# Optimization experiments

Hardware: AMD Instinct MI355X
Metric: run time of the kernel (lower is better)

The kernel has to match this reference:

```python
import jax, jax.numpy as jnp
import numpy as np

N, E, G, D = 100000, 1600000, 1000, 32
EPS = 1e-5


def setup_inputs() -> dict:
    key = jax.random.key(0)
    ks = jax.random.split(key, 24)
    inp = {
        'h': jax.random.normal(ks[0], (N, D), dtype=jnp.float32),
        'src': jax.random.randint(ks[1], (E,), 0, N, dtype=jnp.int32),
        'dst': jax.random.randint(ks[2], (E,), 0, N, dtype=jnp.int32),
        'graph_id': jnp.sort(jax.random.randint(ks[3], (N,), 0, G, dtype=jnp.int32)),
    }
    dims = [D, 32, 32, 32, 1]
    ki = 4
    for i in range(4):
        inp[f'conv_w{i}'] = jax.random.normal(ks[ki], (dims[i], dims[i + 1]), dtype=jnp.float32) * 0.1; ki += 1
        inp[f'conv_b{i}'] = jax.random.normal(ks[ki], (dims[i + 1],), dtype=jnp.float32) * 0.1; ki += 1
        inp[f'bn_g{i}'] = jnp.ones((dims[i + 1],), dtype=jnp.float32)
        inp[f'bn_b{i}'] = jnp.zeros((dims[i + 1],), dtype=jnp.float32)
    mlp_dims = [D + 32 + 32 + 32 + 1, 128, 64, 1]  # 129 -> 128 -> 64 -> 1
    for i in range(3):
        inp[f'mlp_w{i}'] = jax.random.normal(ks[ki], (mlp_dims[i], mlp_dims[i + 1]), dtype=jnp.float32) * 0.1; ki += 1
        inp[f'mlp_b{i}'] = jax.random.normal(ks[ki], (mlp_dims[i + 1],), dtype=jnp.float32) * 0.1; ki += 1
    return inp


def _mean_agg(x, src, dst):
    # DGL update_all(copy_u, mean): h'_v = mean of h_u over in-neighbors u of v
    deg = jax.ops.segment_sum(jnp.ones((src.shape[0],), x.dtype), dst, num_segments=N)
    agg = jax.ops.segment_sum(x[src], dst, num_segments=N)
    return agg / jnp.maximum(deg, 1.0)[:, None]


def _bn(x, g, b):
    # BatchNorm1d in training mode: batch statistics over node dim
    m = x.mean(axis=0)
    v = x.var(axis=0)
    return g * (x - m) * jax.lax.rsqrt(v + EPS) + b


def reference(h, src, dst, graph_id,
              conv_w0, conv_b0, conv_w1, conv_b1, conv_w2, conv_b2, conv_w3, conv_b3,
              bn_g0, bn_b0, bn_g1, bn_b1, bn_g2, bn_b2, bn_g3, bn_b3,
              mlp_w0, mlp_b0, mlp_w1, mlp_b1, mlp_w2, mlp_b2):
    conv = [(conv_w0, conv_b0), (conv_w1, conv_b1), (conv_w2, conv_b2), (conv_w3, conv_b3)]
    bn = [(bn_g0, bn_b0), (bn_g1, bn_b1), (bn_g2, bn_b2), (bn_g3, bn_b3)]
    h_list = [h]
    x = h
    for (w, b), (g, bb) in zip(conv, bn):
        x = _mean_agg(x, src, dst) @ w + b      # GCNConv
        x = jax.nn.relu(_bn(x, g, bb))           # BN + ReLU
        h_list.append(x)
    h_final = jnp.concatenate(h_list, axis=1)    # [N, 129]
    # dgl.mean_nodes: per-graph mean pool
    cnt = jax.ops.segment_sum(jnp.ones((N,), h_final.dtype), graph_id, num_segments=G)
    hg = jax.ops.segment_sum(h_final, graph_id, num_segments=G) / jnp.maximum(cnt, 1.0)[:, None]
    hg = jax.nn.relu(hg @ mlp_w0 + mlp_b0)
    hg = jax.nn.relu(hg @ mlp_w1 + mlp_b1)
    hg = hg @ mlp_w2 + mlp_b2
    return hg.reshape(-1)                         # [G]
```

## Files before the change

kernel.cpp:

```cpp
#include <hip/hip_runtime.h>

#define NSLOT 32
#define BN_EPS 1e-5f
#define NSB 256
#define BKBITS 8
#define BKN 256
#define MAXBUCK 512

static inline int cdiv_h(int a, int b) { return (a + b - 1) / b; }

__device__ __forceinline__ float4 f4add(float4 a, float4 b) {
    return make_float4(a.x + b.x, a.y + b.y, a.z + b.z, a.w + b.w);
}

__device__ __forceinline__ unsigned bf16rtn(float x) {
    unsigned u = __float_as_uint(x);
    return (u + 0x7FFFu + ((u >> 16) & 1u)) >> 16;
}
__device__ __forceinline__ unsigned bf16pack2(float lo, float hi) {
    return bf16rtn(lo) | (bf16rtn(hi) << 16);
}
__device__ __forceinline__ float bfLO(unsigned u) { return __uint_as_float(u << 16); }
__device__ __forceinline__ float bfHI(unsigned u) { return __uint_as_float(u & 0xFFFF0000u); }

__device__ __forceinline__ int blk_excl_scan256(int v, int t) {
    __shared__ int wsum[4];
    int l = t & 63, w = t >> 6;
    int incl = v;
#pragma unroll
    for (int off = 1; off < 64; off <<= 1) {
        int o = __shfl_up(incl, off, 64);
        if (l >= off) incl += o;
    }
    if (l == 63) wsum[w] = incl;
    __syncthreads();
    int wofs = 0;
#pragma unroll
    for (int i = 0; i < 4; i++) wofs += (i < w) ? wsum[i] : 0;
    __syncthreads();
    return wofs + incl - v;
}

__device__ __forceinline__ void bn_coef(const float* __restrict__ sSum, const float* __restrict__ sSq,
                                        const float* __restrict__ bg, const float* __restrict__ bb,
                                        float invN, int ch, float* aOut, float* cOut) {
    float S = 0.f, Q = 0.f;
#pragma unroll
    for (int s = 0; s < NSLOT; s++) { S += sSum[s * 32 + ch]; Q += sSq[s * 32 + ch]; }
    float m = S * invN;
    float var = Q * invN - m * m;
    if (var < 0.f) var = 0.f;
    float iv = rsqrtf(var + BN_EPS);
    float a = bg[ch] * iv;
    *aOut = a;
    *cOut = bb[ch] - m * a;
}

__device__ __forceinline__ void inline_scan512(const int* __restrict__ tot, int* __restrict__ sOut,
                                               int* __restrict__ sTot, int nbuck, int t) {
    int v0 = (t < nbuck) ? tot[t] : 0;
    int v1 = (256 + t < nbuck) ? tot[256 + t] : 0;
    int e0 = blk_excl_scan256(v0, t);
    if (t == 255) *sTot = e0 + v0;
    __syncthreads();
    int e1 = blk_excl_scan256(v1, t) + *sTot;
    sOut[t] = e0;
    sOut[256 + t] = e1;
    __syncthreads();
}

__device__ __forceinline__ void accPlain(float* dst, uint4 v) {
    dst[0] += bfLO(v.x); dst[1] += bfHI(v.x);
    dst[2] += bfLO(v.y); dst[3] += bfHI(v.y);
    dst[4] += bfLO(v.z); dst[5] += bfHI(v.z);
    dst[6] += bfLO(v.w); dst[7] += bfHI(v.w);
}
__device__ __forceinline__ void accAff(float* dst, uint4 v, const float* a8, const float* c8) {
    float x[8] = { bfLO(v.x), bfHI(v.x), bfLO(v.y), bfHI(v.y),
                   bfLO(v.z), bfHI(v.z), bfLO(v.w), bfHI(v.w) };
#pragma unroll
    for (int q = 0; q < 8; q++) { float r = fmaf(a8[q], x[q], c8[q]); dst[q] += r > 0.f ? r : 0.f; }
}

struct KArgs {
    const float* h; const int* src; const int* dst; const int* gid;
    const float* W0; const float* b0c; const float* W1; const float* b1c;
    const float* W2; const float* b2c; const float* w3; const float* b3c;
    const float* bg0; const float* bb0; const float* bg1; const float* bb1;
    const float* bg2; const float* bb2; const float* bg3; const float* bb3;
    const float* mw0; const float* mb0; const float* mw1; const float* mb1;
    const float* mw2; const float* mb2;
    int* histT; int* prefixB; int* totalP; int* totalU;
    unsigned* ebuf; uint4* hb; int* col; int* rs; int* re; int* gstart;
    uint4* y0b; uint4* y1b; uint4* y2b; float* y3;
    float* sSum; float* sSq; float* out;
    int N, E, G, nbuck, chunk, NT64, NT256;
    float invN;
};


__global__ __launch_bounds__(256) void k_p1(KArgs a) {
    __shared__ int bins[MAXBUCK];
    int t = threadIdx.x, bid = blockIdx.x;
    if (bid < NSB) {
        if (bid == 0) {
            for (int i = t; i < 4 * NSLOT * 32; i += 256) { a.sSum[i] = 0.f; a.sSq[i] = 0.f; }
        }
        for (int b = t; b < a.nbuck; b += 256) bins[b] = 0;
        __syncthreads();
        int lo = bid * a.chunk, hi = lo + a.chunk; if (hi > a.E) hi = a.E;
        for (int i = lo + t; i < hi; i += 256) atomicAdd(&bins[a.dst[i] >> BKBITS], 1);
        __syncthreads();
        for (int b = t; b < a.nbuck; b += 256) a.histT[bid * a.nbuck + b] = bins[b];
    } else {
        int node = (bid - NSB) * 256 + t;
        if (node < a.N) {
            const float4* s4 = (const float4*)a.h + (size_t)node * 8;
            float x[32];
#pragma unroll
            for (int q = 0; q < 8; q++) {
                float4 v = s4[q];
                x[4*q] = v.x; x[4*q+1] = v.y; x[4*q+2] = v.z; x[4*q+3] = v.w;
            }
            uint4* d4 = a.hb + (size_t)node * 4;
#pragma unroll
            for (int q = 0; q < 4; q++) {
                uint4 o;
                o.x = bf16pack2(x[8*q+0], x[8*q+1]);
                o.y = bf16pack2(x[8*q+2], x[8*q+3]);
                o.z = bf16pack2(x[8*q+4], x[8*q+5]);
                o.w = bf16pack2(x[8*q+6], x[8*q+7]);
                d4[q] = o;
            }
        }
    }
}


__global__ __launch_bounds__(256) void k_p2(KArgs a) {
    int b = blockIdx.x, t = threadIdx.x;
    int i = b * 256 + t;
    if (i < a.N) {
        int g = a.gid[i];
        int gp = (i == 0) ? -1 : a.gid[i - 1];
        for (int x = gp + 1; x <= g; ++x) a.gstart[x] = i;
        if (i == a.N - 1) { for (int x = g + 1; x <= a.G; ++x) a.gstart[x] = a.N; }
    }
    int c = a.histT[t * a.nbuck + b];
    int pad = (c + 15) & ~15;
    int ep = blk_excl_scan256(pad, t);
    a.prefixB[b * NSB + t] = ep;
    int ec = blk_excl_scan256(c, t);
    if (t == NSB - 1) { a.totalP[b] = ep + pad; a.totalU[b] = ec + c; }
}


__global__ __launch_bounds__(256) void k_p3(KArgs a) {
    __shared__ int sBP[512];
    __shared__ int sTot;
    __shared__ int cur[MAXBUCK];
    int bid = blockIdx.x, t = threadIdx.x;
    inline_scan512(a.totalP, sBP, &sTot, a.nbuck, t);
    for (int b = t; b < a.nbuck; b += 256) cur[b] = sBP[b] + a.prefixB[b * NSB + bid];
    __syncthreads();
    int lo = bid * a.chunk, hi = lo + a.chunk; if (hi > a.E) hi = a.E;
    for (int i = lo + t; i < hi; i += 256) {
        int d = a.dst[i], s = a.src[i];
        int b = d >> BKBITS;
        int pos = atomicAdd(&cur[b], 1);
        a.ebuf[pos] = ((unsigned)(d & (BKN - 1)) << 24) | (unsigned)s;
    }
}


__global__ __launch_bounds__(256) void k_p4(KArgs a) {
    __shared__ int sBP[512];
    __shared__ int sTot;
    __shared__ int binCnt[BKN], binStart[BKN], cursor[BKN];
    __shared__ int cellBase[NSB], cellCnt[NSB];
    int b = blockIdx.x, t = threadIdx.x;
    inline_scan512(a.totalP, sBP, &sTot, a.nbuck, t);
    int basePb = sBP[b];
    __syncthreads();
    inline_scan512(a.totalU, sBP, &sTot, a.nbuck, t);
    int baseUb = sBP[b];
    cellBase[t] = basePb + a.prefixB[b * NSB + t];
    cellCnt[t]  = a.histT[t * a.nbuck + b];
    binCnt[t] = 0; cursor[t] = 0;
    __syncthreads();
    {
        int cb = cellBase[t], cc = cellCnt[t];
        for (int j = 0; j < cc; j++) atomicAdd(&binCnt[a.ebuf[cb + j] >> 24], 1);
    }
    __syncthreads();
    int bs = blk_excl_scan256(binCnt[t], t);
    binStart[t] = bs;
    __syncthreads();
    {
        int cb = cellBase[t], cc = cellCnt[t];
        for (int j = 0; j < cc; j++) {
            unsigned e = a.ebuf[cb + j];
            int l = e >> 24;
            int pos = binStart[l] + atomicAdd(&cursor[l], 1);
            a.col[baseUb + pos] = (int)(e & 0xFFFFFFu);
        }
    }
    int node = b * BKN + t;
    if (node < a.N) {
        a.rs[node] = baseUb + binStart[t];
        a.re[node] = baseUb + binStart[t] + binCnt[t];
    }
}


template <bool AFF>
__device__ __forceinline__ void agg_tile(const KArgs& a, int* scol, float (*sW)[32],
                                         float (*sWS)[32], float (*sWQ)[32], int tile, int t,
                                         const uint4* __restrict__ yin, uint4* __restrict__ yout,
                                         const float* __restrict__ bias, const float* a8, const float* c8,
                                         float* __restrict__ oSum, float* __restrict__ oSq) {
    int lane = t & 3, grp = t >> 2;
    int node0 = tile * 64, node = node0 + grp;
    int base0 = 0, len = 0;
    if (node0 < a.N) {
        int last = node0 + 63; if (last > a.N - 1) last = a.N - 1;
        base0 = a.rs[node0];
        len = a.re[last] - base0;
    }
    bool lds = (len > 0 && len <= 2048);
    if (lds) { for (int i = t; i < len; i += 256) scol[i] = a.col[base0 + i]; }
    __syncthreads();

    float accA[8], accB[8];
#pragma unroll
    for (int q = 0; q < 8; q++) { accA[q] = 0.f; accB[q] = 0.f; }
    float vout[8];
#pragma unroll
    for (int q = 0; q < 8; q++) vout[q] = 0.f;
    int s0 = 0, s1 = 0;
    if (node < a.N) {
        s0 = a.rs[node]; s1 = a.re[node];
#define GATH2(vv, c) vv = yin[(size_t)(c) * 4 + lane]
#define DOACC(d, g) do { if (AFF) accAff(d, g, a8, c8); else accPlain(d, g); } while (0)
        const int* idx = lds ? scol : a.col;
        int j = lds ? s0 - base0 : s0;
        int j1 = lds ? s1 - base0 : s1;
        if (j + 4 <= j1) {
            uint4 g0, g1, g2, g3;
            GATH2(g0, idx[j]); GATH2(g1, idx[j + 1]); GATH2(g2, idx[j + 2]); GATH2(g3, idx[j + 3]);
            j += 4;
            for (; j + 4 <= j1; j += 4) {
                uint4 h0, h1, h2, h3;
                GATH2(h0, idx[j]); GATH2(h1, idx[j + 1]); GATH2(h2, idx[j + 2]); GATH2(h3, idx[j + 3]);
                DOACC(accA, g0); DOACC(accB, g1); DOACC(accA, g2); DOACC(accB, g3);
                g0 = h0; g1 = h1; g2 = h2; g3 = h3;
            }
            DOACC(accA, g0); DOACC(accB, g1); DOACC(accA, g2); DOACC(accB, g3);
        }
        for (; j < j1; ++j) { uint4 g; GATH2(g, idx[j]); DOACC(accA, g); }
#undef GATH2
#undef DOACC
    }
    float* sM = (float*)scol;
    __syncthreads();
    if (node < a.N) {
        int deg = s1 - s0;
        float inv = (deg > 0) ? 1.f / (float)deg : 1.f;
#pragma unroll
        for (int q = 0; q < 8; q++) sM[grp * 33 + lane * 8 + q] = (accA[q] + accB[q]) * inv;
    }
    __syncthreads();
    if (node < a.N) {
        const float4* b4 = (const float4*)bias;
        float4 b0 = b4[lane * 2], b1 = b4[lane * 2 + 1];
        float outv[8] = { b0.x, b0.y, b0.z, b0.w, b1.x, b1.y, b1.z, b1.w };
#pragma unroll
        for (int k = 0; k < 32; k++) {
            float mk = sM[grp * 33 + k];
#pragma unroll
            for (int q = 0; q < 8; q++) outv[q] += mk * sW[k][lane * 8 + q];
        }
#pragma unroll
        for (int q = 0; q < 8; q++) vout[q] = outv[q];
        uint4 o;
        o.x = bf16pack2(vout[0], vout[1]);
        o.y = bf16pack2(vout[2], vout[3]);
        o.z = bf16pack2(vout[4], vout[5]);
        o.w = bf16pack2(vout[6], vout[7]);
        yout[(size_t)node * 4 + lane] = o;
    }
    float sqv[8];
#pragma unroll
    for (int q = 0; q < 8; q++) sqv[q] = vout[q] * vout[q];
#pragma unroll
    for (int off = 4; off < 64; off <<= 1) {
#pragma unroll
        for (int q = 0; q < 8; q++) {
            vout[q] += __shfl_xor(vout[q], off, 64);
            sqv[q]  += __shfl_xor(sqv[q],  off, 64);
        }
    }
    int w = t >> 6, l = t & 63;
    if (l < 4) {
#pragma unroll
        for (int q = 0; q < 8; q++) { sWS[w][l * 8 + q] = vout[q]; sWQ[w][l * 8 + q] = sqv[q]; }
    }
    __syncthreads();
    if (t < 32) {
        float S = sWS[0][t] + sWS[1][t] + sWS[2][t] + sWS[3][t];
        float Q = sWQ[0][t] + sWQ[1][t] + sWQ[2][t] + sWQ[3][t];
        int slot = tile & (NSLOT - 1);
        atomicAdd(&oSum[slot * 32 + t], S);
        atomicAdd(&oSq[slot * 32 + t], Q);
    }
}


__global__ __launch_bounds__(256, 4) void k_p5(KArgs a) {
    __shared__ int scol[2112];
    __shared__ float sW[32][32];
    __shared__ float sWS[4][32];
    __shared__ float sWQ[4][32];
    int t = threadIdx.x;
    for (int i = t; i < 1024; i += 256) sW[i >> 5][i & 31] = a.W0[i];
    __syncthreads();
    agg_tile<false>(a, scol, sW, sWS, sWQ, blockIdx.x, t, a.hb, a.y0b, a.b0c, nullptr, nullptr,
                    a.sSum + 0 * NSLOT * 32, a.sSq + 0 * NSLOT * 32);
}


__device__ __forceinline__ void aggF_kernel(const KArgs& a, const uint4* yin, uint4* yout,
                                            const float* W, const float* bias,
                                            const float* pSum, const float* pSq,
                                            const float* bg, const float* bb,
                                            float* oSum, float* oSq) {
    __shared__ int scol[2112];
    __shared__ float sW[32][32];
    __shared__ float sA[32], sC[32];
    __shared__ float sWS[4][32];
    __shared__ float sWQ[4][32];
    int t = threadIdx.x;
    for (int i = t; i < 1024; i += 256) sW[i >> 5][i & 31] = W[i];
    if (t < 32) bn_coef(pSum, pSq, bg, bb, a.invN, t, &sA[t], &sC[t]);
    __syncthreads();
    float a8[8], c8[8];
    int lane = t & 3;
#pragma unroll
    for (int q = 0; q < 8; q++) { a8[q] = sA[lane * 8 + q]; c8[q] = sC[lane * 8 + q]; }
    agg_tile<true>(a, scol, sW, sWS, sWQ, blockIdx.x, t, yin, yout, bias, a8, c8, oSum, oSq);
}

__global__ __launch_bounds__(256, 4) void k_p6(KArgs a) {
    aggF_kernel(a, a.y0b, a.y1b, a.W1, a.b1c,
                a.sSum + 0 * NSLOT * 32, a.sSq + 0 * NSLOT * 32, a.bg0, a.bb0,
                a.sSum + 1 * NSLOT * 32, a.sSq + 1 * NSLOT * 32);
}
__global__ __launch_bounds__(256, 4) void k_p7(KArgs a) {
    aggF_kernel(a, a.y1b, a.y2b, a.W2, a.b2c,
                a.sSum + 1 * NSLOT * 32, a.sSq + 1 * NSLOT * 32, a.bg1, a.bb1,
                a.sSum + 2 * NSLOT * 32, a.sSq + 2 * NSLOT * 32);
}


__global__ __launch_bounds__(256) void k_p8(KArgs a) {
    __shared__ float sw[32], sA[32], sC[32];
    int t = threadIdx.x;
    float* q = (float*)a.hb;
    if (t < 32) {
        sw[t] = a.w3[t];
        bn_coef(a.sSum + 2 * NSLOT * 32, a.sSq + 2 * NSLOT * 32, a.bg2, a.bb2,
                a.invN, t, &sA[t], &sC[t]);
    }
    __syncthreads();
    int i = blockIdx.x * 256 + t;
    if (i < a.N) {
        const uint4* x4 = a.y2b + (size_t)i * 4;
        float acc = 0.f;
#pragma unroll
        for (int qq = 0; qq < 4; qq++) {
            uint4 u = x4[qq];
            float vv[8] = { bfLO(u.x), bfHI(u.x), bfLO(u.y), bfHI(u.y),
                            bfLO(u.z), bfHI(u.z), bfLO(u.w), bfHI(u.w) };
#pragma unroll
            for (int r = 0; r < 8; r++) {
                int k = qq * 8 + r;
                float xv = sA[k] * vv[r] + sC[k];
                xv = xv > 0.f ? xv : 0.f;
                acc += xv * sw[k];
            }
        }
        q[i] = acc;
    }
}


__global__ __launch_bounds__(256) void k_p9(KArgs a) {
    __shared__ float sWS3[4], sWQ3[4];
    const float* q = (const float*)a.hb;
    int t = threadIdx.x;
    int i = blockIdx.x * 256 + t;
    float lsum = 0.f, lsq = 0.f;
    if (i < a.N) {
        int s0 = a.rs[i], s1 = a.re[i];
        float a0 = 0.f, a1 = 0.f, a2 = 0.f, a3 = 0.f;
        int j = s0;
        if (j + 4 <= s1) {
            float g0 = q[a.col[j]], g1 = q[a.col[j+1]], g2 = q[a.col[j+2]], g3 = q[a.col[j+3]];
            j += 4;
            for (; j + 4 <= s1; j += 4) {
                float h0 = q[a.col[j]], h1 = q[a.col[j+1]], h2 = q[a.col[j+2]], h3 = q[a.col[j+3]];
                a0 += g0; a1 += g1; a2 += g2; a3 += g3;
                g0 = h0; g1 = h1; g2 = h2; g3 = h3;
            }
            a0 += g0; a1 += g1; a2 += g2; a3 += g3;
        }
        for (; j < s1; ++j) a0 += q[a.col[j]];
        float acc = (a0 + a1) + (a2 + a3);
        float inv = (s1 > s0) ? 1.f / (float)(s1 - s0) : 1.f;
        float v = acc * inv + a.b3c[0];
        a.y3[i] = v; lsum = v; lsq = v * v;
    }
#pragma unroll
    for (int off = 1; off < 64; off <<= 1) {
        lsum += __shfl_xor(lsum, off, 64);
        lsq  += __shfl_xor(lsq,  off, 64);
    }
    if ((t & 63) == 0) { sWS3[t >> 6] = lsum; sWQ3[t >> 6] = lsq; }
    __syncthreads();
    if (t == 0) {
        float S = sWS3[0] + sWS3[1] + sWS3[2] + sWS3[3];
        float Q = sWQ3[0] + sWQ3[1] + sWQ3[2] + sWQ3[3];
        int slot = blockIdx.x & (NSLOT - 1);
        atomicAdd(&a.sSum[3 * NSLOT * 32 + slot * 32], S);
        atomicAdd(&a.sSq[3 * NSLOT * 32 + slot * 32], Q);
    }
}


__global__ __launch_bounds__(256) void k_p10(KArgs a) {
    __shared__ float pcA[128], pcC[128];
    __shared__ float sP[8][128];
    __shared__ float sY[4];
    __shared__ float hg[129];
    __shared__ float hid1[128];
    __shared__ float hid2[64];
    int g = blockIdx.x;
    int t = threadIdx.x;
    if (t < 97) {
        int layer = (t == 96) ? 3 : (t >> 5);
        int ch = t & 31;
        const float* bg = (layer == 0) ? a.bg0 : (layer == 1) ? a.bg1 : (layer == 2) ? a.bg2 : a.bg3;
        const float* bb = (layer == 0) ? a.bb0 : (layer == 1) ? a.bb1 : (layer == 2) ? a.bb2 : a.bb3;
        bn_coef(a.sSum + layer * NSLOT * 32, a.sSq + layer * NSLOT * 32, bg, bb, a.invN, ch,
                &pcA[t], &pcC[t]);
    }
    __syncthreads();
    int s0 = a.gstart[g], s1 = a.gstart[g + 1];
    int lane = t & 31, slot = t >> 5;
    int arr = lane >> 3, sub = lane & 7;
    const unsigned* yb = (arr == 1) ? (const unsigned*)a.y0b
                       : (arr == 2) ? (const unsigned*)a.y1b : (const unsigned*)a.y2b;
    float4 a4 = make_float4(1.f, 1.f, 1.f, 1.f);
    float4 c4 = make_float4(0.f, 0.f, 0.f, 0.f);
    bool aff = (arr > 0);
    if (aff) {
        a4 = ((const float4*)pcA)[(arr - 1) * 8 + sub];
        c4 = ((const float4*)pcC)[(arr - 1) * 8 + sub];
    }
    float4 acc = make_float4(0.f, 0.f, 0.f, 0.f);
    for (int n = s0 + slot; n < s1; n += 8) {
        float4 v;
        if (arr == 0) {
            v = ((const float4*)a.h)[(size_t)n * 8 + sub];
        } else {
            uint2 u = ((const uint2*)yb)[(size_t)n * 8 + sub];
            v = make_float4(bfLO(u.x), bfHI(u.x), bfLO(u.y), bfHI(u.y));
        }
        if (aff) {
            float vx = fmaf(a4.x, v.x, c4.x); vx = vx > 0.f ? vx : 0.f;
            float vy = fmaf(a4.y, v.y, c4.y); vy = vy > 0.f ? vy : 0.f;
            float vz = fmaf(a4.z, v.z, c4.z); vz = vz > 0.f ? vz : 0.f;
            float vw = fmaf(a4.w, v.w, c4.w); vw = vw > 0.f ? vw : 0.f;
            v = make_float4(vx, vy, vz, vw);
        }
        acc = f4add(acc, v);
    }
    float ys = 0.f;
    {
        float aY = pcA[96], cY = pcC[96];
        for (int n = s0 + t; n < s1; n += 256) {
            float v = fmaf(aY, a.y3[n], cY);
            ys += v > 0.f ? v : 0.f;
        }
    }
#pragma unroll
    for (int off = 1; off < 64; off <<= 1) ys += __shfl_xor(ys, off, 64);
    if ((t & 63) == 0) sY[t >> 6] = ys;
    ((float4*)&sP[slot][lane * 4])[0] = acc;
    __syncthreads();
    float inv = (s1 > s0) ? 1.f / (float)(s1 - s0) : 1.f;
    if (t < 128) {
        float S = 0.f;
#pragma unroll
        for (int s = 0; s < 8; s++) S += sP[s][t];
        hg[t] = S * inv;
    } else if (t == 128) {
        float S = sY[0] + sY[1] + sY[2] + sY[3];
        hg[128] = S * inv;
    }
    __syncthreads();
    if (t < 128) {
        float v = a.mb0[t];
        for (int i = 0; i < 129; i++) v += hg[i] * a.mw0[i * 128 + t];
        hid1[t] = v > 0.f ? v : 0.f;
    }
    __syncthreads();
    if (t < 64) {
        float v = a.mb1[t];
        for (int i = 0; i < 128; i++) v += hid1[i] * a.mw1[i * 64 + t];
        hid2[t] = v > 0.f ? v : 0.f;
    }
    __syncthreads();
    if (t < 64) {
        float v = hid2[t] * a.mw2[t];
        for (int off = 32; off > 0; off >>= 1) v += __shfl_down(v, off, 64);
        if (t == 0) a.out[g] = v + a.mb2[0];
    }
}


extern "C" void kernel_launch(void* const* d_in, const int* in_sizes, int n_in,
                              void* d_out, int out_size, void* d_ws, size_t ws_size,
                              hipStream_t stream) {
    KArgs ka;
    ka.h   = (const float*)d_in[0];
    ka.src = (const int*)d_in[1];
    ka.dst = (const int*)d_in[2];
    ka.gid = (const int*)d_in[3];
    const float* convw[4], *convb[4], *bng[4], *bnb[4];
    for (int i = 0; i < 4; i++) {
        convw[i] = (const float*)d_in[4 + 4 * i];
        convb[i] = (const float*)d_in[5 + 4 * i];
        bng[i]   = (const float*)d_in[6 + 4 * i];
        bnb[i]   = (const float*)d_in[7 + 4 * i];
    }
    ka.W0 = convw[0]; ka.b0c = convb[0]; ka.W1 = convw[1]; ka.b1c = convb[1];
    ka.W2 = convw[2]; ka.b2c = convb[2]; ka.w3 = convw[3]; ka.b3c = convb[3];
    ka.bg0 = bng[0]; ka.bb0 = bnb[0]; ka.bg1 = bng[1]; ka.bb1 = bnb[1];
    ka.bg2 = bng[2]; ka.bb2 = bnb[2]; ka.bg3 = bng[3]; ka.bb3 = bnb[3];
    ka.mw0 = (const float*)d_in[20]; ka.mb0 = (const float*)d_in[21];
    ka.mw1 = (const float*)d_in[22]; ka.mb1 = (const float*)d_in[23];
    ka.mw2 = (const float*)d_in[24]; ka.mb2 = (const float*)d_in[25];

    const int N = in_sizes[0] / 32;
    const int E = in_sizes[1];
    const int G = out_size;
    const int nbuck = cdiv_h(N, BKN);
    const int chunk = cdiv_h(E, NSB);

    char* ws = (char*)d_ws;
    size_t off = 0;
    auto alloc = [&](size_t bytes) -> void* {
        void* p = ws + off;
        off += (bytes + 511) & ~(size_t)511;
        return p;
    };
    ka.histT   = (int*)alloc((size_t)NSB * nbuck * 4);
    ka.prefixB = (int*)alloc((size_t)nbuck * NSB * 4);
    ka.totalP  = (int*)alloc((size_t)nbuck * 4);
    ka.totalU  = (int*)alloc((size_t)nbuck * 4);
    size_t ebufE = (size_t)E + (size_t)16 * NSB * nbuck;
    ka.ebuf = (unsigned*)alloc(ebufE * 4);
    ka.hb   = (uint4*)alloc((size_t)N * 64);
    ka.col  = (int*)alloc((size_t)E * 4);
    ka.rs   = (int*)alloc((size_t)N * 4);
    ka.re   = (int*)alloc((size_t)N * 4);
    ka.gstart = (int*)alloc((size_t)(G + 1) * 4);
    ka.y0b  = (uint4*)alloc((size_t)N * 64);
    ka.y1b  = (uint4*)alloc((size_t)N * 64);
    ka.y2b  = (uint4*)alloc((size_t)N * 64);
    ka.y3   = (float*)alloc((size_t)N * 4);
    ka.sSum = (float*)alloc((size_t)4 * NSLOT * 32 * 4);
    ka.sSq  = (float*)alloc((size_t)4 * NSLOT * 32 * 4);
    ka.out  = (float*)d_out;
    (void)ws_size; (void)n_in;

    ka.N = N; ka.E = E; ka.G = G; ka.nbuck = nbuck; ka.chunk = chunk;
    ka.NT64 = cdiv_h(N, 64); ka.NT256 = cdiv_h(N, 256);
    ka.invN = 1.f / (float)N;

    k_p1<<<NSB + ka.NT256, 256, 0, stream>>>(ka);
    k_p2<<<nbuck, 256, 0, stream>>>(ka);
    k_p3<<<NSB, 256, 0, stream>>>(ka);
    k_p4<<<nbuck, 256, 0, stream>>>(ka);
    k_p5<<<ka.NT64, 256, 0, stream>>>(ka);
    k_p6<<<ka.NT64, 256, 0, stream>>>(ka);
    k_p7<<<ka.NT64, 256, 0, stream>>>(ka);
    k_p8<<<ka.NT256, 256, 0, stream>>>(ka);
    k_p9<<<ka.NT256, 256, 0, stream>>>(ka);
    k_p10<<<G, 256, 0, stream>>>(ka);
}
```

Baseline: 294.6 us.

## Apply first-layer weight before aggregation and specialize layer-0 kernel

Uses linearity of mean aggregation to compute h@W0 per node in the bf16 conversion pass, so the first aggregation kernel only gathers pre-projected features, adds bias and skips its shared-memory matmul. The agg_tile template is inlined into separate kernels, and occupancy hints are raised (layer 0 to 6 blocks, layers 1-2 to 5). This removes a 32x32 matmul and two barriers from the gather-bound layer-0 kernel, at the cost of a per-node matmul in the prep kernel and bf16 rounding applied after the projection instead of before.

```diff
diff --git a/kernel.cpp b/kernel.cpp
--- a/kernel.cpp
+++ b/kernel.cpp
@@ -91,7 +91,7 @@
     const float* mw0; const float* mb0; const float* mw1; const float* mb1;
     const float* mw2; const float* mb2;
     int* histT; int* prefixB; int* totalP; int* totalU;
-    unsigned* ebuf; uint4* hb; int* col; int* rs; int* re; int* gstart;
+    unsigned* ebuf; uint4* pb; int* col; int* rs; int* re; int* gstart;
     uint4* y0b; uint4* y1b; uint4* y2b; float* y3;
     float* sSum; float* sSq; float* out;
     int N, E, G, nbuck, chunk, NT64, NT256;
@@ -101,6 +101,7 @@
 
 __global__ __launch_bounds__(256) void k_p1(KArgs a) {
     __shared__ int bins[MAXBUCK];
+    __shared__ float sW[32][32];
     int t = threadIdx.x, bid = blockIdx.x;
     if (bid < NSB) {
         if (bid == 0) {
@@ -113,25 +114,35 @@
         __syncthreads();
         for (int b = t; b < a.nbuck; b += 256) a.histT[bid * a.nbuck + b] = bins[b];
     } else {
+        for (int i = t; i < 1024; i += 256) sW[i >> 5][i & 31] = a.W0[i];
+        __syncthreads();
         int node = (bid - NSB) * 256 + t;
-        if (node < a.N) {
-            const float4* s4 = (const float4*)a.h + (size_t)node * 8;
-            float x[32];
-#pragma unroll
-            for (int q = 0; q < 8; q++) {
-                float4 v = s4[q];
-                x[4*q] = v.x; x[4*q+1] = v.y; x[4*q+2] = v.z; x[4*q+3] = v.w;
-            }
-            uint4* d4 = a.hb + (size_t)node * 4;
-#pragma unroll
-            for (int q = 0; q < 4; q++) {
-                uint4 o;
-                o.x = bf16pack2(x[8*q+0], x[8*q+1]);
-                o.y = bf16pack2(x[8*q+2], x[8*q+3]);
-                o.z = bf16pack2(x[8*q+4], x[8*q+5]);
-                o.w = bf16pack2(x[8*q+6], x[8*q+7]);
-                d4[q] = o;
-            }
+        if (node >= a.N) return;
+        float x[32];
+        const float4* s4 = (const float4*)a.h + (size_t)node * 8;
+#pragma unroll
+        for (int q = 0; q < 8; q++) {
+            float4 v = s4[q];
+            x[4*q] = v.x; x[4*q+1] = v.y; x[4*q+2] = v.z; x[4*q+3] = v.w;
+        }
+        float acc[32];
+#pragma unroll
+        for (int f = 0; f < 32; f++) acc[f] = 0.f;
+#pragma unroll
+        for (int k = 0; k < 32; k++) {
+            float xv = x[k];
+#pragma unroll
+            for (int f = 0; f < 32; f++) acc[f] += xv * sW[k][f];
+        }
+        uint4* d4 = a.pb + (size_t)node * 4;
+#pragma unroll
+        for (int q = 0; q < 4; q++) {
+            uint4 o;
+            o.x = bf16pack2(acc[8*q+0], acc[8*q+1]);
+            o.y = bf16pack2(acc[8*q+2], acc[8*q+3]);
+            o.z = bf16pack2(acc[8*q+4], acc[8*q+5]);
+            o.w = bf16pack2(acc[8*q+6], acc[8*q+7]);
+            d4[q] = o;
         }
     }
 }
@@ -213,14 +224,13 @@
 }
 
 
-template <bool AFF>
-__device__ __forceinline__ void agg_tile(const KArgs& a, int* scol, float (*sW)[32],
-                                         float (*sWS)[32], float (*sWQ)[32], int tile, int t,
-                                         const uint4* __restrict__ yin, uint4* __restrict__ yout,
-                                         const float* __restrict__ bias, const float* a8, const float* c8,
-                                         float* __restrict__ oSum, float* __restrict__ oSq) {
+__global__ __launch_bounds__(256, 6) void k_p5(KArgs a) {
+    __shared__ int scol[2048];
+    __shared__ float sWS[4][32];
+    __shared__ float sWQ[4][32];
+    int t = threadIdx.x;
     int lane = t & 3, grp = t >> 2;
-    int node0 = tile * 64, node = node0 + grp;
+    int node0 = blockIdx.x * 64, node = node0 + grp;
     int base0 = 0, len = 0;
     if (node0 < a.N) {
         int last = node0 + 63; if (last > a.N - 1) last = a.N - 1;
@@ -237,11 +247,9 @@
     float vout[8];
 #pragma unroll
     for (int q = 0; q < 8; q++) vout[q] = 0.f;
-    int s0 = 0, s1 = 0;
     if (node < a.N) {
-        s0 = a.rs[node]; s1 = a.re[node];
-#define GATH2(vv, c) vv = yin[(size_t)(c) * 4 + lane]
-#define DOACC(d, g) do { if (AFF) accAff(d, g, a8, c8); else accPlain(d, g); } while (0)
+        int s0 = a.rs[node], s1 = a.re[node];
+#define GATH2(vv, c) vv = a.pb[(size_t)(c) * 4 + lane]
         const int* idx = lds ? scol : a.col;
         int j = lds ? s0 - base0 : s0;
         int j1 = lds ? s1 - base0 : s1;
@@ -252,42 +260,31 @@
             for (; j + 4 <= j1; j += 4) {
                 uint4 h0, h1, h2, h3;
                 GATH2(h0, idx[j]); GATH2(h1, idx[j + 1]); GATH2(h2, idx[j + 2]); GATH2(h3, idx[j + 3]);
-                DOACC(accA, g0); DOACC(accB, g1); DOACC(accA, g2); DOACC(accB, g3);
+                accPlain(accA, g0); accPlain(accB, g1); accPlain(accA, g2); accPlain(accB, g3);
                 g0 = h0; g1 = h1; g2 = h2; g3 = h3;
             }
-            DOACC(accA, g0); DOACC(accB, g1); DOACC(accA, g2); DOACC(accB, g3);
-        }
-        for (; j < j1; ++j) { uint4 g; GATH2(g, idx[j]); DOACC(accA, g); }
+            accPlain(accA, g0); accPlain(accB, g1); accPlain(accA, g2); accPlain(accB, g3);
+        }
+        for (; j < j1; ++j) { uint4 g; GATH2(g, idx[j]); accPlain(accA, g); }
 #undef GATH2
-#undef DOACC
-    }
-    float* sM = (float*)scol;
-    __syncthreads();
-    if (node < a.N) {
         int deg = s1 - s0;
         float inv = (deg > 0) ? 1.f / (float)deg : 1.f;
-#pragma unroll
-        for (int q = 0; q < 8; q++) sM[grp * 33 + lane * 8 + q] = (accA[q] + accB[q]) * inv;
-    }
-    __syncthreads();
-    if (node < a.N) {
-        const float4* b4 = (const float4*)bias;
+        const float4* b4 = (const float4*)a.b0c;
         float4 b0 = b4[lane * 2], b1 = b4[lane * 2 + 1];
-        float outv[8] = { b0.x, b0.y, b0.z, b0.w, b1.x, b1.y, b1.z, b1.w };
-#pragma unroll
-        for (int k = 0; k < 32; k++) {
-            float mk = sM[grp * 33 + k];
-#pragma unroll
-            for (int q = 0; q < 8; q++) outv[q] += mk * sW[k][lane * 8 + q];
-        }
-#pragma unroll
-        for (int q = 0; q < 8; q++) vout[q] = outv[q];
+        vout[0] = (accA[0] + accB[0]) * inv + b0.x;
+        vout[1] = (accA[1] + accB[1]) * inv + b0.y;
+        vout[2] = (accA[2] + accB[2]) * inv + b0.z;
+        vout[3] = (accA[3] + accB[3]) * inv + b0.w;
+        vout[4] = (accA[4] + accB[4]) * inv + b1.x;
+        vout[5] = (accA[5] + accB[5]) * inv + b1.y;
+        vout[6] = (accA[6] + accB[6]) * inv + b1.z;
+        vout[7] = (accA[7] + accB[7]) * inv + b1.w;
         uint4 o;
         o.x = bf16pack2(vout[0], vout[1]);
         o.y = bf16pack2(vout[2], vout[3]);
         o.z = bf16pack2(vout[4], vout[5]);
         o.w = bf16pack2(vout[6], vout[7]);
-        yout[(size_t)node * 4 + lane] = o;
+        a.y0b[(size_t)node * 4 + lane] = o;
     }
     float sqv[8];
 #pragma unroll
@@ -309,23 +306,10 @@
     if (t < 32) {
         float S = sWS[0][t] + sWS[1][t] + sWS[2][t] + sWS[3][t];
         float Q = sWQ[0][t] + sWQ[1][t] + sWQ[2][t] + sWQ[3][t];
-        int slot = tile & (NSLOT - 1);
-        atomicAdd(&oSum[slot * 32 + t], S);
-        atomicAdd(&oSq[slot * 32 + t], Q);
-    }
-}
-
-
-__global__ __launch_bounds__(256, 4) void k_p5(KArgs a) {
-    __shared__ int scol[2112];
-    __shared__ float sW[32][32];
-    __shared__ float sWS[4][32];
-    __shared__ float sWQ[4][32];
-    int t = threadIdx.x;
-    for (int i = t; i < 1024; i += 256) sW[i >> 5][i & 31] = a.W0[i];
-    __syncthreads();
-    agg_tile<false>(a, scol, sW, sWS, sWQ, blockIdx.x, t, a.hb, a.y0b, a.b0c, nullptr, nullptr,
-                    a.sSum + 0 * NSLOT * 32, a.sSq + 0 * NSLOT * 32);
+        int slot = blockIdx.x & (NSLOT - 1);
+        atomicAdd(&a.sSum[slot * 32 + t], S);
+        atomicAdd(&a.sSq[slot * 32 + t], Q);
+    }
 }
 
 
@@ -342,20 +326,112 @@
     int t = threadIdx.x;
     for (int i = t; i < 1024; i += 256) sW[i >> 5][i & 31] = W[i];
     if (t < 32) bn_coef(pSum, pSq, bg, bb, a.invN, t, &sA[t], &sC[t]);
+    int lane = t & 3, grp = t >> 2;
+    int node0 = blockIdx.x * 64, node = node0 + grp;
+    int base0 = 0, len = 0;
+    if (node0 < a.N) {
+        int last = node0 + 63; if (last > a.N - 1) last = a.N - 1;
+        base0 = a.rs[node0];
+        len = a.re[last] - base0;
+    }
+    bool lds = (len > 0 && len <= 2048);
+    __syncthreads();
+    if (lds) { for (int i = t; i < len; i += 256) scol[i] = a.col[base0 + i]; }
     __syncthreads();
     float a8[8], c8[8];
-    int lane = t & 3;
 #pragma unroll
     for (int q = 0; q < 8; q++) { a8[q] = sA[lane * 8 + q]; c8[q] = sC[lane * 8 + q]; }
-    agg_tile<true>(a, scol, sW, sWS, sWQ, blockIdx.x, t, yin, yout, bias, a8, c8, oSum, oSq);
-}
-
-__global__ __launch_bounds__(256, 4) void k_p6(KArgs a) {
+
+    float accA[8], accB[8];
+#pragma unroll
+    for (int q = 0; q < 8; q++) { accA[q] = 0.f; accB[q] = 0.f; }
+    float vout[8];
+#pragma unroll
+    for (int q = 0; q < 8; q++) vout[q] = 0.f;
+    int s0 = 0, s1 = 0;
+    if (node < a.N) {
+        s0 = a.rs[node]; s1 = a.re[node];
+#define GATH2(vv, c) vv = yin[(size_t)(c) * 4 + lane]
+        const int* idx = lds ? scol : a.col;
+        int j = lds ? s0 - base0 : s0;
+        int j1 = lds ? s1 - base0 : s1;
+        if (j + 4 <= j1) {
+            uint4 g0, g1, g2, g3;
+            GATH2(g0, idx[j]); GATH2(g1, idx[j + 1]); GATH2(g2, idx[j + 2]); GATH2(g3, idx[j + 3]);
+            j += 4;
+            for (; j + 4 <= j1; j += 4) {
+                uint4 h0, h1, h2, h3;
+                GATH2(h0, idx[j]); GATH2(h1, idx[j + 1]); GATH2(h2, idx[j + 2]); GATH2(h3, idx[j + 3]);
+                accAff(accA, g0, a8, c8); accAff(accB, g1, a8, c8);
+                accAff(accA, g2, a8, c8); accAff(accB, g3, a8, c8);
+                g0 = h0; g1 = h1; g2 = h2; g3 = h3;
+            }
+            accAff(accA, g0, a8, c8); accAff(accB, g1, a8, c8);
+            accAff(accA, g2, a8, c8); accAff(accB, g3, a8, c8);
+        }
+        for (; j < j1; ++j) { uint4 g; GATH2(g, idx[j]); accAff(accA, g, a8, c8); }
+#undef GATH2
+    }
+    float* sM = (float*)scol;
+    __syncthreads();
+    if (node < a.N) {
+        int deg = s1 - s0;
+        float inv = (deg > 0) ? 1.f / (float)deg : 1.f;
+#pragma unroll
+        for (int q = 0; q < 8; q++) sM[grp * 33 + lane * 8 + q] = (accA[q] + accB[q]) * inv;
+    }
+    __syncthreads();
+    if (node < a.N) {
+        const float4* b4 = (const float4*)bias;
+        float4 b0 = b4[lane * 2], b1 = b4[lane * 2 + 1];
+        float outv[8] = { b0.x, b0.y, b0.z, b0.w, b1.x, b1.y, b1.z, b1.w };
+#pragma unroll
+        for (int k = 0; k < 32; k++) {
+            float mk = sM[grp * 33 + k];
+#pragma unroll
+            for (int q = 0; q < 8; q++) outv[q] += mk * sW[k][lane * 8 + q];
+        }
+#pragma unroll
+        for (int q = 0; q < 8; q++) vout[q] = outv[q];
+        uint4 o;
+        o.x = bf16pack2(vout[0], vout[1]);
+        o.y = bf16pack2(vout[2], vout[3]);
+        o.z = bf16pack2(vout[4], vout[5]);
+        o.w = bf16pack2(vout[6], vout[7]);
+        yout[(size_t)node * 4 + lane] = o;
+    }
+    float sqv[8];
+#pragma unroll
+    for (int q = 0; q < 8; q++) sqv[q] = vout[q] * vout[q];
+#pragma unroll
+    for (int off = 4; off < 64; off <<= 1) {
+#pragma unroll
+        for (int q = 0; q < 8; q++) {
+            vout[q] += __shfl_xor(vout[q], off, 64);
+            sqv[q]  += __shfl_xor(sqv[q],  off, 64);
+        }
+    }
+    int w = t >> 6, l = t & 63;
+    if (l < 4) {
+#pragma unroll
+        for (int q = 0; q < 8; q++) { sWS[w][l * 8 + q] = vout[q]; sWQ[w][l * 8 + q] = sqv[q]; }
+    }
+    __syncthreads();
+    if (t < 32) {
+        float S = sWS[0][t] + sWS[1][t] + sWS[2][t] + sWS[3][t];
+        float Q = sWQ[0][t] + sWQ[1][t] + sWQ[2][t] + sWQ[3][t];
+        int slot = blockIdx.x & (NSLOT - 1);
+        atomicAdd(&oSum[slot * 32 + t], S);
+        atomicAdd(&oSq[slot * 32 + t], Q);
+    }
+}
+
+__global__ __launch_bounds__(256, 5) void k_p6(KArgs a) {
     aggF_kernel(a, a.y0b, a.y1b, a.W1, a.b1c,
                 a.sSum + 0 * NSLOT * 32, a.sSq + 0 * NSLOT * 32, a.bg0, a.bb0,
                 a.sSum + 1 * NSLOT * 32, a.sSq + 1 * NSLOT * 32);
 }
-__global__ __launch_bounds__(256, 4) void k_p7(KArgs a) {
+__global__ __launch_bounds__(256, 5) void k_p7(KArgs a) {
     aggF_kernel(a, a.y1b, a.y2b, a.W2, a.b2c,
                 a.sSum + 1 * NSLOT * 32, a.sSq + 1 * NSLOT * 32, a.bg1, a.bb1,
                 a.sSum + 2 * NSLOT * 32, a.sSq + 2 * NSLOT * 32);
@@ -365,7 +441,7 @@
 __global__ __launch_bounds__(256) void k_p8(KArgs a) {
     __shared__ float sw[32], sA[32], sC[32];
     int t = threadIdx.x;
-    float* q = (float*)a.hb;
+    float* q = (float*)a.pb;
     if (t < 32) {
         sw[t] = a.w3[t];
         bn_coef(a.sSum + 2 * NSLOT * 32, a.sSq + 2 * NSLOT * 32, a.bg2, a.bb2,
@@ -396,7 +472,7 @@
 
 __global__ __launch_bounds__(256) void k_p9(KArgs a) {
     __shared__ float sWS3[4], sWQ3[4];
-    const float* q = (const float*)a.hb;
+    const float* q = (const float*)a.pb;
     int t = threadIdx.x;
     int i = blockIdx.x * 256 + t;
     float lsum = 0.f, lsq = 0.f;
@@ -571,7 +647,7 @@
     ka.totalU  = (int*)alloc((size_t)nbuck * 4);
     size_t ebufE = (size_t)E + (size_t)16 * NSB * nbuck;
     ka.ebuf = (unsigned*)alloc(ebufE * 4);
-    ka.hb   = (uint4*)alloc((size_t)N * 64);
+    ka.pb   = (uint4*)alloc((size_t)N * 64);
     ka.col  = (int*)alloc((size_t)E * 4);
     ka.rs   = (int*)alloc((size_t)N * 4);
     ka.re   = (int*)alloc((size_t)N * 4);
```

After: 283.5 us (median of 2 runs). 1.04x faster.
